# Optimization experiments

Measured on AMD Instinct MI355X. Metric: run time of the kernel, lower is better.

## Reference

```python
import jax, jax.numpy as jnp
import numpy as np

N = 16384          # batch
K = 4096           # num_neurons per LogicLayer
L = 4              # num_layers
IN0 = 4            # first layer in_dim (= 2*D from cat([x,-x]))
CLASSES = 2
TAU = 1.0


def setup_inputs() -> dict:
    key = jax.random.key(0)
    k1, k2, k3 = jax.random.split(key, 3)
    rng = np.random.default_rng(0)
    x = jax.random.normal(k1, (N, 2), dtype=jnp.float32)
    w0 = jax.random.normal(k2, (K, 16), dtype=jnp.float32)
    ws = jax.random.normal(k3, (L - 1, K, 16), dtype=jnp.float32)
    ia0 = jnp.asarray(rng.integers(0, IN0, size=(K,)), dtype=jnp.int32)
    ib0 = jnp.asarray(rng.integers(0, IN0, size=(K,)), dtype=jnp.int32)
    ia = jnp.asarray(rng.integers(0, K, size=(L - 1, K)), dtype=jnp.int32)
    ib = jnp.asarray(rng.integers(0, K, size=(L - 1, K)), dtype=jnp.int32)
    return dict(x=x, w0=w0, ws=ws, ia0=ia0, ib0=ib0, ia=ia, ib=ib)


def logic_layer(h, w, idx_a, idx_b):
    """Differentiable logic layer (difflogic, training mode).

    out = sum_i softmax(w)_i * op_i(a, b) over the 16 two-input boolean
    functions. All 16 ops are multilinear in (a, b), so the weighted sum
    collapses exactly to c0 + ca*a + cb*b + cab*a*b with per-neuron coeffs.
    """
    p = jax.nn.softmax(w, axis=-1)  # [k, 16]
    a = h[:, idx_a]                 # [N, k]
    b = h[:, idx_b]                 # [N, k]
    ca = p[:, 2] + p[:, 3] + p[:, 6] + p[:, 7] - p[:, 8] - p[:, 9] - p[:, 12] - p[:, 13]
    cb = p[:, 4] + p[:, 5] + p[:, 6] + p[:, 7] - p[:, 8] - p[:, 9] - p[:, 10] - p[:, 11]
    cab = (p[:, 1] - p[:, 2] - p[:, 4] - 2.0 * p[:, 6] - p[:, 7]
           + p[:, 8] + 2.0 * p[:, 9] + p[:, 11] + p[:, 13] - p[:, 14])
    c0 = p[:, 8] + p[:, 9] + p[:, 10] + p[:, 11] + p[:, 12] + p[:, 13] + p[:, 14] + p[:, 15]
    return c0 + ca * a + cb * b + cab * (a * b)


def _model(iv, w0, ws, ia0, ib0, ia, ib):
    h = logic_layer(iv, w0, ia0, ib0)
    for l in range(ws.shape[0]):  # small fixed layer loop
        h = logic_layer(h, ws[l], ia[l], ib[l])
    # GroupSum(class_count=2, tau=1.0)
    return h.reshape(h.shape[0], CLASSES, -1).sum(-1) / TAU


def reference(x, w0, ws, ia0, ib0, ia, ib):
    mx = jnp.concatenate([x, -x], axis=1)  # [N, 4]
    thresh_space = 0.5

    # ---- ti = 0: thresh = 0, flags all zero -> input_values = tx ----
    tx = (mx > 0.0).astype(jnp.float32)
    iv = tx
    rt0 = _model(iv, w0, ws, ia0, ib0, ia, ib)          # [N, 2]
    # flags[n,d,o] = 1 where input_values[n,d] != results[n,0,o]
    flags = (iv[:, :, None] != rt0[:, None, :]).astype(jnp.float32)  # [N, 4, 2]

    # ---- ti = 1 ----
    lastl = jnp.argmax(rt0, axis=1)                      # [N]
    wadj = jnp.where(lastl > 0, thresh_space, -thresh_space)
    thresh = wadj                                        # started from zeros
    tx = (mx > thresh[:, None]).astype(jnp.float32)
    # nested oi-loop writes tx wherever flags[n,d,oi]==0 for any oi
    upd = jnp.any(flags == 0.0, axis=2)                  # [N, 4]
    iv = jnp.where(upd, tx, iv)
    rt1 = _model(iv, w0, ws, ia0, ib0, ia, ib)           # [N, 2]
    return rt1
```

## Files before the change

### kernel.cpp

```cpp
#include <hip/hip_runtime.h>
#include <hip/hip_fp16.h>

#define KN 4096
#define NSAMP 16384


__device__ __forceinline__ void softmax16(const float* __restrict__ wp,
                                          float& c0, float& ca, float& cb, float& cab) {
    const float4* wr = (const float4*)wp;
    float4 v0 = wr[0], v1 = wr[1], v2 = wr[2], v3 = wr[3];
    float e0 = __expf(v0.x), e1 = __expf(v0.y), e2 = __expf(v0.z), e3 = __expf(v0.w);
    float e4 = __expf(v1.x), e5 = __expf(v1.y), e6 = __expf(v1.z), e7 = __expf(v1.w);
    float e8 = __expf(v2.x), e9 = __expf(v2.y), e10 = __expf(v2.z), e11 = __expf(v2.w);
    float e12 = __expf(v3.x), e13 = __expf(v3.y), e14 = __expf(v3.z), e15 = __expf(v3.w);
    float s = ((e0 + e1) + (e2 + e3)) + ((e4 + e5) + (e6 + e7))
            + ((e8 + e9) + (e10 + e11)) + ((e12 + e13) + (e14 + e15));
    float can  = ((e2 + e3) + (e6 + e7)) - ((e8 + e9) + (e12 + e13));
    float cbn  = ((e4 + e5) + (e6 + e7)) - ((e8 + e9) + (e10 + e11));
    float cabn = (e1 - e2) - (e4 + e7) - 2.0f * e6 + (e8 + e11) + 2.0f * e9
               + (e13 - e14);
    float c0n  = ((e8 + e9) + (e10 + e11)) + ((e12 + e13) + (e14 + e15));
    float inv = 1.0f / s;
    c0 = c0n * inv; ca = can * inv; cb = cbn * inv; cab = cabn * inv;
}

__global__ __launch_bounds__(256) void prep(
    const float* __restrict__ w0, const float* __restrict__ wsG,
    const int* __restrict__ ia0, const int* __restrict__ ib0,
    const int* __restrict__ ia, const int* __restrict__ ib,
    const float* __restrict__ x,
    uint2* __restrict__ cf16, unsigned* __restrict__ pidx,
    float* __restrict__ h0all, unsigned char* __restrict__ pats) {
    const int bid = blockIdx.x, tid = threadIdx.x;
    if (bid < 48) {
        int g = KN + bid * 256 + tid;
        int layer = g >> 12;
        int k = g & 4095;
        float c0, ca, cb, cab;
        softmax16(wsG + ((size_t)(layer - 1) * KN + k) * 16, c0, ca, cb, cab);
        __half2 p01 = __floats2half2_rn(c0, ca);
        __half2 p23 = __floats2half2_rn(cb, cab);
        uint2 c;
        c.x = *(unsigned*)&p01;
        c.y = *(unsigned*)&p23;
        cf16[g] = c;
        pidx[g] = (unsigned)ia[(layer - 1) * KN + k]
                | ((unsigned)ib[(layer - 1) * KN + k] << 16);
    } else if (bid < 304) {
        int j = (bid - 48) * 256 + tid;
        int pat = j >> 12, k = j & 4095;
        float c0, ca, cb, cab;
        softmax16(w0 + (size_t)k * 16, c0, ca, cb, cab);
        float a = (float)((pat >> ia0[k]) & 1);
        float b = (float)((pat >> ib0[k]) & 1);
        h0all[j] = c0 + ca * a + cb * b + cab * (a * b);
    } else {
        int n = (bid - 304) * 256 + tid;
        float2 xv = ((const float2*)x)[n];
        int p0 = (int)(xv.x > 0.0f) | ((int)(xv.y > 0.0f) << 1)
               | ((int)(-xv.x > 0.0f) << 2) | ((int)(-xv.y > 0.0f) << 3);
        pats[n] = (unsigned char)p0;
    }
}

__device__ __forceinline__ float neuron2(uint2 c, float a, float b) {
    float2 c01 = __half22float2(*(__half2*)&c.x);
    float2 c23 = __half22float2(*(__half2*)&c.y);
    return c01.x + c01.y * a + c23.x * b + c23.y * (a * b);
}

__device__ void eval_full(int pp, const uint2* __restrict__ cf16,
                          const unsigned* __restrict__ pidx,
                          const float* __restrict__ h0all,
                          float* h0, float* h1, float* red, int tid,
                          float& r0, float& r1) {
    #pragma unroll
    for (int i = 0; i < 4; ++i) {
        int k = tid + i * 1024;
        h0[k] = h0all[pp * KN + k];
    }
    __syncthreads();
    for (int l = 1; l <= 3; ++l) {
        const float* src = (l & 1) ? h0 : h1;
        float* dst = (l & 1) ? h1 : h0;
        #pragma unroll
        for (int i = 0; i < 4; ++i) {
            int k = tid + i * 1024;
            unsigned xi = pidx[l * KN + k];
            dst[k] = neuron2(cf16[l * KN + k], src[xi & 0xffff], src[xi >> 16]);
        }
        __syncthreads();
    }
    float s0 = h1[tid] + h1[tid + 1024];
    float s1 = h1[tid + 2048] + h1[tid + 3072];
    #pragma unroll
    for (int off = 32; off > 0; off >>= 1) {
        s0 += __shfl_down(s0, off, 64);
        s1 += __shfl_down(s1, off, 64);
    }
    int wid = tid >> 6, lane = tid & 63;
    if (lane == 0) { red[wid] = s0; red[16 + wid] = s1; }
    __syncthreads();
    if (tid == 0) {
        float t0 = 0.0f, t1 = 0.0f;
        #pragma unroll
        for (int wq = 0; wq < 16; ++wq) { t0 += red[wq]; t1 += red[16 + wq]; }
        red[32] = t0; red[33] = t1;
    }
    __syncthreads();
    r0 = red[32]; r1 = red[33];
    __syncthreads();
}

__global__ __launch_bounds__(1024) void table_scatter(
    const uint2* __restrict__ cf16, const unsigned* __restrict__ pidx,
    const float* __restrict__ h0all, const unsigned char* __restrict__ pats,
    const float* __restrict__ x, float* __restrict__ out) {
    __shared__ float h0[KN];
    __shared__ float h1[KN];
    __shared__ float red[34];
    __shared__ float tbl[32];
    const int pat = blockIdx.x;
    const int tid = threadIdx.x;

    uint2 cB[4], cA[4];
    unsigned xB[4], xA[4];
    #pragma unroll
    for (int i = 0; i < 4; ++i) {
        int k = tid + i * 1024;
        cB[i] = cf16[KN + k];      xB[i] = pidx[KN + k];
        cA[i] = cf16[2 * KN + k];  xA[i] = pidx[2 * KN + k];
    }
    #pragma unroll
    for (int i = 0; i < 4; ++i) {
        int k = tid + i * 1024;
        h0[k] = h0all[pat * KN + k];
    }
    __syncthreads();

    #pragma unroll
    for (int i = 0; i < 4; ++i) {
        int k = tid + i * 1024;
        h1[k] = neuron2(cB[i], h0[xB[i] & 0xffff], h0[xB[i] >> 16]);
        cB[i] = cf16[3 * KN + k];
        xB[i] = pidx[3 * KN + k];
    }
    __syncthreads();
    #pragma unroll
    for (int i = 0; i < 4; ++i) {
        int k = tid + i * 1024;
        h0[k] = neuron2(cA[i], h1[xA[i] & 0xffff], h1[xA[i] >> 16]);
    }
    __syncthreads();
    float s0 = 0.0f, s1 = 0.0f;
    #pragma unroll
    for (int i = 0; i < 4; ++i) {
        float o = neuron2(cB[i], h0[xB[i] & 0xffff], h0[xB[i] >> 16]);
        if (i < 2) s0 += o; else s1 += o;
    }
    #pragma unroll
    for (int off = 32; off > 0; off >>= 1) {
        s0 += __shfl_down(s0, off, 64);
        s1 += __shfl_down(s1, off, 64);
    }
    int wid = tid >> 6, lane = tid & 63;
    if (lane == 0) { red[wid] = s0; red[16 + wid] = s1; }
    __syncthreads();
    if (tid == 0) {
        float t0 = 0.0f, t1 = 0.0f;
        #pragma unroll
        for (int wq = 0; wq < 16; ++wq) { t0 += red[wq]; t1 += red[16 + wq]; }
        red[32] = t0; red[33] = t1;
    }
    __syncthreads();
    float r0 = red[32], r1 = red[33];

    bool slow = (r0 == 0.0f) || (r0 == 1.0f) || (r1 == 0.0f) || (r1 == 1.0f);
    if (!slow) {
        uint4 pv = ((const uint4*)pats)[tid];
        int base = tid * 16;
        unsigned wv[4] = { pv.x, pv.y, pv.z, pv.w };
        #pragma unroll
        for (int wq = 0; wq < 4; ++wq) {
            #pragma unroll
            for (int b = 0; b < 4; ++b) {
                if (((wv[wq] >> (8 * b)) & 0xffu) == (unsigned)pat) {
                    int n = base + wq * 4 + b;
                    ((float2*)out)[n] = make_float2(r0, r1);
                }
            }
        }
    } else {
        for (int pp = 0; pp < 16; ++pp) {
            float q0, q1;
            eval_full(pp, cf16, pidx, h0all, h0, h1, red, tid, q0, q1);
            if (tid == 0) { tbl[2 * pp] = q0; tbl[2 * pp + 1] = q1; }
        }
        __syncthreads();
        for (int n = tid; n < NSAMP; n += 1024) {
            if (pats[n] != (unsigned char)pat) continue;
            float2 xv = ((const float2*)x)[n];
            float mx[4] = { xv.x, xv.y, -xv.x, -xv.y };
            float ivf[4];
            int p0 = 0;
            #pragma unroll
            for (int i = 0; i < 4; ++i) {
                int b = mx[i] > 0.0f;
                ivf[i] = (float)b;
                p0 |= b << i;
            }
            float q0 = tbl[2 * p0], q1 = tbl[2 * p0 + 1];
            int lastl = (q1 > q0) ? 1 : 0;
            float thresh = lastl ? 0.5f : -0.5f;
            int p1 = 0;
            #pragma unroll
            for (int i = 0; i < 4; ++i) {
                bool upd = (ivf[i] == q0) || (ivf[i] == q1);
                int bit = upd ? (int)(mx[i] > thresh) : (int)ivf[i];
                p1 |= bit << i;
            }
            ((float2*)out)[n] = make_float2(tbl[2 * p1], tbl[2 * p1 + 1]);
        }
    }
}

extern "C" void kernel_launch(void* const* d_in, const int* in_sizes, int n_in,
                              void* d_out, int out_size, void* d_ws, size_t ws_size,
                              hipStream_t stream) {
    const float* x   = (const float*)d_in[0];
    const float* w0  = (const float*)d_in[1];
    const float* wsG = (const float*)d_in[2];
    const int* ia0   = (const int*)d_in[3];
    const int* ib0   = (const int*)d_in[4];
    const int* ia    = (const int*)d_in[5];
    const int* ib    = (const int*)d_in[6];

    uint2* cf16         = (uint2*)d_ws;
    unsigned* pidx      = (unsigned*)((char*)d_ws + 131072);
    float* h0all        = (float*)((char*)d_ws + 196608);
    unsigned char* pats = (unsigned char*)d_ws + 458752;

    prep<<<368, 256, 0, stream>>>(w0, wsG, ia0, ib0, ia, ib, x,
                                  cf16, pidx, h0all, pats);
    table_scatter<<<16, 1024, 0, stream>>>(cf16, pidx, h0all, pats, x,
                                           (float*)d_out);
}
```

Before: 17.32 us.

## Skip absent input patterns, store layer-0 table in fp16, fold pattern loop into prep

```diff
diff --git a/kernel.cpp b/kernel.cpp
--- a/kernel.cpp
+++ b/kernel.cpp
@@ -30,7 +30,8 @@
     const int* __restrict__ ia, const int* __restrict__ ib,
     const float* __restrict__ x,
     uint2* __restrict__ cf16, unsigned* __restrict__ pidx,
-    float* __restrict__ h0all, unsigned char* __restrict__ pats) {
+    __half* __restrict__ h0f16, unsigned char* __restrict__ pats,
+    unsigned* __restrict__ maskp) {
     const int bid = blockIdx.x, tid = threadIdx.x;
     if (bid < 48) {
         int g = KN + bid * 256 + tid;
@@ -46,20 +47,31 @@
         cf16[g] = c;
         pidx[g] = (unsigned)ia[(layer - 1) * KN + k]
                 | ((unsigned)ib[(layer - 1) * KN + k] << 16);
-    } else if (bid < 304) {
-        int j = (bid - 48) * 256 + tid;
-        int pat = j >> 12, k = j & 4095;
+    } else if (bid < 64) {
+        int k = (bid - 48) * 256 + tid;
         float c0, ca, cb, cab;
         softmax16(w0 + (size_t)k * 16, c0, ca, cb, cab);
-        float a = (float)((pat >> ia0[k]) & 1);
-        float b = (float)((pat >> ib0[k]) & 1);
-        h0all[j] = c0 + ca * a + cb * b + cab * (a * b);
+        int A = ia0[k], B = ib0[k];
+        #pragma unroll
+        for (int pat = 0; pat < 16; ++pat) {
+            float a = (float)((pat >> A) & 1);
+            float b = (float)((pat >> B) & 1);
+            h0f16[pat * KN + k] = __float2half(c0 + ca * a + cb * b + cab * (a * b));
+        }
     } else {
-        int n = (bid - 304) * 256 + tid;
+        int n = (bid - 64) * 256 + tid;
         float2 xv = ((const float2*)x)[n];
         int p0 = (int)(xv.x > 0.0f) | ((int)(xv.y > 0.0f) << 1)
                | ((int)(-xv.x > 0.0f) << 2) | ((int)(-xv.y > 0.0f) << 3);
         pats[n] = (unsigned char)p0;
+        __shared__ unsigned sm[4];
+        unsigned m = 1u << p0;
+        #pragma unroll
+        for (int off = 32; off > 0; off >>= 1) m |= __shfl_xor(m, off, 64);
+        int wid = tid >> 6, lane = tid & 63;
+        if (lane == 0) sm[wid] = m;
+        __syncthreads();
+        if (tid == 0) maskp[bid - 64] = sm[0] | sm[1] | sm[2] | sm[3];
     }
 }
 
@@ -71,13 +83,13 @@
 
 __device__ void eval_full(int pp, const uint2* __restrict__ cf16,
                           const unsigned* __restrict__ pidx,
-                          const float* __restrict__ h0all,
+                          const __half* __restrict__ h0f16,
                           float* h0, float* h1, float* red, int tid,
                           float& r0, float& r1) {
     #pragma unroll
     for (int i = 0; i < 4; ++i) {
         int k = tid + i * 1024;
-        h0[k] = h0all[pp * KN + k];
+        h0[k] = __half2float(h0f16[pp * KN + k]);
     }
     __syncthreads();
     for (int l = 1; l <= 3; ++l) {
@@ -114,15 +126,26 @@
 
 __global__ __launch_bounds__(1024) void table_scatter(
     const uint2* __restrict__ cf16, const unsigned* __restrict__ pidx,
-    const float* __restrict__ h0all, const unsigned char* __restrict__ pats,
+    const __half* __restrict__ h0f16, const unsigned char* __restrict__ pats,
+    const unsigned* __restrict__ maskp,
     const float* __restrict__ x, float* __restrict__ out) {
     __shared__ float h0[KN];
     __shared__ float h1[KN];
     __shared__ float red[34];
     __shared__ float tbl[32];
+    __shared__ unsigned smask;
     const int pat = blockIdx.x;
     const int tid = threadIdx.x;
 
+    if (tid < 64) {
+        unsigned m = maskp[tid];
+        #pragma unroll
+        for (int off = 32; off > 0; off >>= 1) m |= __shfl_xor(m, off, 64);
+        if (tid == 0) smask = m;
+    }
+    __syncthreads();
+    if (!((smask >> pat) & 1u)) return;
+
     uint2 cB[4], cA[4];
     unsigned xB[4], xA[4];
     #pragma unroll
@@ -131,10 +154,13 @@
         cB[i] = cf16[KN + k];      xB[i] = pidx[KN + k];
         cA[i] = cf16[2 * KN + k];  xA[i] = pidx[2 * KN + k];
     }
-    #pragma unroll
-    for (int i = 0; i < 4; ++i) {
-        int k = tid + i * 1024;
-        h0[k] = h0all[pat * KN + k];
+    {
+        uint2 hv = ((const uint2*)(h0f16 + pat * KN))[tid];
+        float2 lo = __half22float2(*(__half2*)&hv.x);
+        float2 hi = __half22float2(*(__half2*)&hv.y);
+        int k = tid * 4;
+        h0[k + 0] = lo.x; h0[k + 1] = lo.y;
+        h0[k + 2] = hi.x; h0[k + 3] = hi.y;
     }
     __syncthreads();
 
@@ -193,7 +219,7 @@
     } else {
         for (int pp = 0; pp < 16; ++pp) {
             float q0, q1;
-            eval_full(pp, cf16, pidx, h0all, h0, h1, red, tid, q0, q1);
+            eval_full(pp, cf16, pidx, h0f16, h0, h1, red, tid, q0, q1);
             if (tid == 0) { tbl[2 * pp] = q0; tbl[2 * pp + 1] = q1; }
         }
         __syncthreads();
@@ -237,11 +263,12 @@
 
     uint2* cf16         = (uint2*)d_ws;
     unsigned* pidx      = (unsigned*)((char*)d_ws + 131072);
-    float* h0all        = (float*)((char*)d_ws + 196608);
-    unsigned char* pats = (unsigned char*)d_ws + 458752;
-
-    prep<<<368, 256, 0, stream>>>(w0, wsG, ia0, ib0, ia, ib, x,
-                                  cf16, pidx, h0all, pats);
-    table_scatter<<<16, 1024, 0, stream>>>(cf16, pidx, h0all, pats, x,
+    __half* h0f16       = (__half*)((char*)d_ws + 196608);
+    unsigned char* pats = (unsigned char*)d_ws + 327680;
+    unsigned* maskp     = (unsigned*)((char*)d_ws + 344064);
+
+    prep<<<128, 256, 0, stream>>>(w0, wsG, ia0, ib0, ia, ib, x,
+                                  cf16, pidx, h0f16, pats, maskp);
+    table_scatter<<<16, 1024, 0, stream>>>(cf16, pidx, h0f16, pats, maskp, x,
                                            (float*)d_out);
 }
```

After: 18.13 us. 1.05x slower.
